# Optimization experiments

Hardware: AMD Instinct MI355X
Metric: run time of the kernel (lower is better)

## Reference

```python
import jax, jax.numpy as jnp
import numpy as np

N_NODES = 50000
N_EDGES = 800000
N_GRAPHS = 64
D_IN = 128
D_HID = 128
D_OUT = 32
N_LAYERS = 2


def setup_inputs() -> dict:
    key = jax.random.key(0)
    ks = jax.random.split(key, 12)
    x = jax.random.normal(ks[0], (N_NODES, D_IN), dtype=jnp.float32)
    edge_index = jax.random.randint(ks[1], (2, N_EDGES), 0, N_NODES, dtype=jnp.int64)
    batch = jnp.sort(jax.random.randint(ks[2], (N_NODES,), 0, N_GRAPHS, dtype=jnp.int64))
    s = 1.0 / np.sqrt(D_HID)
    return {
        "x": x,
        "edge_index": edge_index,
        "batch": batch,
        "conv_w_rel": jax.random.normal(ks[3], (N_LAYERS, D_IN, D_HID), dtype=jnp.float32) * s,
        "conv_b_rel": jax.random.normal(ks[4], (N_LAYERS, D_HID), dtype=jnp.float32) * s,
        "conv_w_root": jax.random.normal(ks[5], (N_LAYERS, D_IN, D_HID), dtype=jnp.float32) * s,
        "sage_w_l": jax.random.normal(ks[6], (N_LAYERS, D_HID, D_HID), dtype=jnp.float32) * s,
        "sage_b_l": jax.random.normal(ks[7], (N_LAYERS, D_HID), dtype=jnp.float32) * s,
        "sage_w_r": jax.random.normal(ks[8], (N_LAYERS, D_HID, D_HID), dtype=jnp.float32) * s,
        "fc_w": jax.random.normal(ks[9], (D_HID, D_OUT), dtype=jnp.float32) * s,
        "fc_b": jax.random.normal(ks[10], (D_OUT,), dtype=jnp.float32) * s,
    }


def reference(x, edge_index, batch, conv_w_rel, conv_b_rel, conv_w_root,
              sage_w_l, sage_b_l, sage_w_r, fc_w, fc_b):
    N = x.shape[0]
    src, dst = edge_index[0], edge_index[1]
    # StandardScaler: per-feature standardization (population std)
    mu = jnp.mean(x, axis=0)
    sd = jnp.std(x, axis=0)
    h = (x - mu) / sd
    # Stacked GraphConv layers: lin_rel(sum-aggr neighbors) + lin_root(x), then ReLU
    for l in range(conv_w_rel.shape[0]):
        agg = jax.ops.segment_sum(h[src], dst, num_segments=N)  # [N, D]
        h = jax.nn.relu(agg @ conv_w_rel[l] + conv_b_rel[l] + h @ conv_w_root[l])
    # GraphSAGE: SAGEConv layers (mean aggregation), ReLU between layers only
    deg = jax.ops.segment_sum(jnp.ones((src.shape[0],), dtype=h.dtype), dst, num_segments=N)
    deg = jnp.clip(deg, 1.0)[:, None]  # [N, 1]
    L = sage_w_l.shape[0]
    for l in range(L):
        agg = jax.ops.segment_sum(h[src], dst, num_segments=N) / deg  # mean over neighbors
        h_new = agg @ sage_w_l[l] + sage_b_l[l] + h @ sage_w_r[l]
        h = jax.nn.relu(h_new) if l < L - 1 else h_new
    # global_mean_pool over graphs
    sums = jax.ops.segment_sum(h, batch, num_segments=N_GRAPHS)  # [G, D]
    cnt = jax.ops.segment_sum(jnp.ones((N,), dtype=h.dtype), batch, num_segments=N_GRAPHS)
    pooled = sums / jnp.clip(cnt, 1.0)[:, None]
    return pooled @ fc_w + fc_b  # [G, D_OUT]
```

## Files before the change

kernel.cpp:

```cpp
#include <hip/hip_runtime.h>

#define N_NODES 50000
#define N_EDGES 800000
#define N_GRAPHS 64
#define DH 128
#define DOUT 32

typedef __attribute__((ext_vector_type(8))) short bf16x8;
typedef __attribute__((ext_vector_type(4))) float f32x4;

__device__ __forceinline__ unsigned short f2bf(float f) {
    union { float f; unsigned int u; } x;
    x.f = f;
    unsigned int u = x.u;
    u += 0x7FFFu + ((u >> 16) & 1u);
    return (unsigned short)(u >> 16);
}

#define STAT_BLKS 512
__global__ __launch_bounds__(256) void stats_kernel(const float* __restrict__ x,
                                                    float* __restrict__ partial) {
    __shared__ float4 shs[256];
    __shared__ float4 shq[256];
    const int tid = threadIdx.x;
    const int rowgrp = tid >> 5;
    const int cq = tid & 31;
    float4 s = make_float4(0.f, 0.f, 0.f, 0.f);
    float4 q = make_float4(0.f, 0.f, 0.f, 0.f);
#pragma unroll 4
    for (int r = blockIdx.x * 8 + rowgrp; r < N_NODES; r += STAT_BLKS * 8) {
        const float4 v = *reinterpret_cast<const float4*>(x + (size_t)r * DH + cq * 4);
        s.x += v.x; s.y += v.y; s.z += v.z; s.w += v.w;
        q.x = fmaf(v.x, v.x, q.x); q.y = fmaf(v.y, v.y, q.y);
        q.z = fmaf(v.z, v.z, q.z); q.w = fmaf(v.w, v.w, q.w);
    }
    shs[tid] = s; shq[tid] = q;
    __syncthreads();
    for (int off = 128; off >= 32; off >>= 1) {
        if (tid < off) {
            float4 a = shs[tid], b = shs[tid + off];
            a.x += b.x; a.y += b.y; a.z += b.z; a.w += b.w;
            shs[tid] = a;
            float4 c = shq[tid], d = shq[tid + off];
            c.x += d.x; c.y += d.y; c.z += d.z; c.w += d.w;
            shq[tid] = c;
        }
        __syncthreads();
    }
    if (tid < 32) {
        const float4 a = shs[tid];
        const float4 c = shq[tid];
        const float sv[4] = {a.x, a.y, a.z, a.w};
        const float qv[4] = {c.x, c.y, c.z, c.w};
#pragma unroll
        for (int j = 0; j < 4; ++j) {
            const int col = tid * 4 + j;
            partial[(size_t)col * STAT_BLKS + blockIdx.x] = sv[j];
            partial[(size_t)(128 + col) * STAT_BLKS + blockIdx.x] = qv[j];
        }
    }
}

__global__ __launch_bounds__(128) void finalize_stats_kernel(const float* __restrict__ partial,
                                                             float* __restrict__ stat) {
    const int c = threadIdx.x;
    const float4* ps = reinterpret_cast<const float4*>(partial + (size_t)c * STAT_BLKS);
    const float4* pq = reinterpret_cast<const float4*>(partial + (size_t)(128 + c) * STAT_BLKS);
    float s = 0.f, q = 0.f;
#pragma unroll 8
    for (int b = 0; b < STAT_BLKS / 4; ++b) {
        const float4 v = ps[b];
        s += v.x + v.y + v.z + v.w;
        const float4 w = pq[b];
        q += w.x + w.y + w.z + w.w;
    }
    const float inv_n = 1.0f / (float)N_NODES;
    const float mu = s * inv_n;
    const float var = q * inv_n - mu * mu;
    const float sd = sqrtf(fmaxf(var, 1e-20f));
    stat[256 + c] = mu;
    stat[384 + c] = 1.0f / sd;
}

__global__ void standardize_kernel(const float* __restrict__ x,
                                   const float* __restrict__ stat,
                                   unsigned short* __restrict__ h) {
    const size_t i = (size_t)blockIdx.x * blockDim.x + threadIdx.x;
    const int c4 = (int)(i & 31) << 2;
    const float4 v = reinterpret_cast<const float4*>(x)[i];
    const float4 m = *reinterpret_cast<const float4*>(stat + 256 + c4);
    const float4 is = *reinterpret_cast<const float4*>(stat + 384 + c4);
    ushort4 o;
    o.x = f2bf((v.x - m.x) * is.x);
    o.y = f2bf((v.y - m.y) * is.y);
    o.z = f2bf((v.z - m.z) * is.z);
    o.w = f2bf((v.w - m.w) * is.w);
    reinterpret_cast<ushort4*>(h)[i] = o;
}

__global__ void count_deg_kernel(const int* __restrict__ dst, int* __restrict__ deg_i) {
    int e = blockIdx.x * blockDim.x + threadIdx.x;
    if (e < N_EDGES) atomicAdd(&deg_i[dst[e]], 1);
}

#define SCAN_BLK 256
#define SCAN_NBLK ((N_NODES + SCAN_BLK - 1) / SCAN_BLK)

__global__ __launch_bounds__(SCAN_BLK) void scan_local_kernel(const int* __restrict__ deg_i,
                                                              int* __restrict__ row_ptr,
                                                              int* __restrict__ bsum) {
    __shared__ int sh[SCAN_BLK];
    const int tid = threadIdx.x;
    const int idx = blockIdx.x * SCAN_BLK + tid;
    const int v = (idx < N_NODES) ? deg_i[idx] : 0;
    sh[tid] = v;
    __syncthreads();
#pragma unroll
    for (int off = 1; off < SCAN_BLK; off <<= 1) {
        const int t = (tid >= off) ? sh[tid - off] : 0;
        __syncthreads();
        sh[tid] += t;
        __syncthreads();
    }
    if (idx < N_NODES) row_ptr[idx] = sh[tid] - v;
    if (tid == SCAN_BLK - 1) bsum[blockIdx.x] = sh[tid];
}

__global__ __launch_bounds__(SCAN_BLK) void scan_bsum_kernel(int* __restrict__ bsum) {
    __shared__ int sh[SCAN_BLK];
    const int tid = threadIdx.x;
    const int v = (tid < SCAN_NBLK) ? bsum[tid] : 0;
    sh[tid] = v;
    __syncthreads();
#pragma unroll
    for (int off = 1; off < SCAN_BLK; off <<= 1) {
        const int t = (tid >= off) ? sh[tid - off] : 0;
        __syncthreads();
        sh[tid] += t;
        __syncthreads();
    }
    if (tid < SCAN_NBLK) bsum[tid] = sh[tid] - v;
}

__global__ __launch_bounds__(SCAN_BLK) void scan_finalize_kernel(const int* __restrict__ deg_i,
                                                                 const int* __restrict__ bsum,
                                                                 int* __restrict__ row_ptr,
                                                                 int* __restrict__ cursor,
                                                                 float* __restrict__ deg_inv) {
    const int tid = threadIdx.x;
    const int idx = blockIdx.x * SCAN_BLK + tid;
    if (idx < N_NODES) {
        const int excl = row_ptr[idx] + bsum[blockIdx.x];
        row_ptr[idx] = excl;
        cursor[idx] = excl;
        const int d = deg_i[idx];
        deg_inv[idx] = 1.0f / (float)(d > 1 ? d : 1);
    }
    if (idx == 0) row_ptr[N_NODES] = N_EDGES;
}

#define NXCD 8
#define RANGE_NODES ((N_NODES + NXCD - 1) / NXCD)
#define SC_SLICES 104
__global__ __launch_bounds__(256) void scatter_ranged_kernel(const int* __restrict__ src,
                                                             const int* __restrict__ dst,
                                                             int* __restrict__ cursor,
                                                             int* __restrict__ csr_src) {
    const int range = blockIdx.x & (NXCD - 1);
    const int slice = blockIdx.x >> 3;
    const int lo = range * RANGE_NODES;
    const int hi = min(lo + RANGE_NODES, N_NODES);
    const int stride = SC_SLICES * 256;
    for (int e = slice * 256 + threadIdx.x; e < N_EDGES; e += stride) {
        const int d = dst[e];
        if (d >= lo && d < hi) {
            const int pos = atomicAdd(&cursor[d], 1);
            csr_src[pos] = src[e];
        }
    }
}

__global__ __launch_bounds__(256) void aggregate_csr_kernel(const unsigned short* __restrict__ h,
                                                            const int* __restrict__ row_ptr,
                                                            const int* __restrict__ csr_src,
                                                            const float* __restrict__ deg_inv,
                                                            unsigned short* __restrict__ agg,
                                                            const int useScale) {
    const int node = blockIdx.x * 4 + (threadIdx.x >> 6);
    if (node >= N_NODES) return;
    const int lane = threadIdx.x & 63;
    const int beg = row_ptr[node];
    const int end = row_ptr[node + 1];
    float a0 = 0.f, a1 = 0.f;
    for (int chunk = beg; chunk < end; chunk += 64) {
        const int cnt = min(64, end - chunk);
        const int sv = (lane < cnt) ? csr_src[chunk + lane] : 0;
        int j = 0;
        for (; j + 8 <= cnt; j += 8) {
            int ss[8];
#pragma unroll
            for (int u = 0; u < 8; ++u) ss[u] = __shfl(sv, j + u);
            unsigned int vv[8];
#pragma unroll
            for (int u = 0; u < 8; ++u)
                vv[u] = *reinterpret_cast<const unsigned int*>(h + (size_t)ss[u] * DH + lane * 2);
#pragma unroll
            for (int u = 0; u < 8; ++u) {
                union { unsigned int x; float f; } t;
                t.x = vv[u] << 16; a0 += t.f;
                t.x = vv[u] & 0xFFFF0000u; a1 += t.f;
            }
        }
        for (; j < cnt; ++j) {
            const int s = __shfl(sv, j);
            const unsigned int v = *reinterpret_cast<const unsigned int*>(h + (size_t)s * DH + lane * 2);
            union { unsigned int x; float f; } t;
            t.x = v << 16; a0 += t.f;
            t.x = v & 0xFFFF0000u; a1 += t.f;
        }
    }
    float o0 = a0, o1 = a1;
    if (useScale) {
        const float sc = deg_inv[node];
        o0 *= sc; o1 *= sc;
    }
    const unsigned int packed = (unsigned int)f2bf(o0) | ((unsigned int)f2bf(o1) << 16);
    reinterpret_cast<unsigned int*>(agg + (size_t)node * DH)[lane] = packed;
}

__global__ void pack_w_kernel(const float* __restrict__ cwr, const float* __restrict__ cwroot,
                              const float* __restrict__ swl, const float* __restrict__ swr,
                              unsigned short* __restrict__ wfrag) {
    const int g = blockIdx.x * blockDim.x + threadIdx.x;
    if (g >= 16384) return;
    const int lane = g & 63;
    const int n = (g >> 6) & 7;
    const int t = (g >> 9) & 3;
    const int phase = (g >> 11) & 1;
    const int layer = (g >> 12) & 3;
    const float* W1 = (layer < 2) ? (cwr + layer * 16384) : (swl + (layer - 2) * 16384);
    const float* W2 = (layer < 2) ? (cwroot + layer * 16384) : (swr + (layer - 2) * 16384);
    const float* W = phase ? W2 : W1;
    const int col = n * 16 + (lane & 15);
    const int k0 = t * 32 + (lane >> 4) * 8;
    unsigned short v[8];
#pragma unroll
    for (int j = 0; j < 8; ++j) v[j] = f2bf(W[(size_t)(k0 + j) * DH + col]);
    unsigned short* dstp = wfrag + ((size_t)g * 8);
#pragma unroll
    for (int j = 0; j < 8; ++j) dstp[j] = v[j];
}

__global__ __launch_bounds__(256) void fused_layer_mfma_kernel(
    const unsigned short* __restrict__ A1, const unsigned short* __restrict__ A2,
    const unsigned short* __restrict__ Wf, const float* __restrict__ bias,
    unsigned short* __restrict__ Cb, float* __restrict__ Cf, const int relu) {
    const int wid = threadIdx.x >> 6;
    const int lane = threadIdx.x & 63;
    const int row0 = blockIdx.x * 64 + wid * 16;
    const int arow = row0 + (lane & 15);
    const int koff = (lane >> 4) * 8;
    const bool rowOK = (arow < N_NODES);

    f32x4 acc[8];
#pragma unroll
    for (int n = 0; n < 8; ++n) acc[n] = (f32x4){0.f, 0.f, 0.f, 0.f};

#pragma unroll
    for (int phase = 0; phase < 2; ++phase) {
        const unsigned short* Ar = (phase ? A2 : A1) + (size_t)arow * DH;
        const unsigned short* Wp = Wf + (size_t)phase * (4 * 8 * 64 * 8);
#pragma unroll
        for (int t = 0; t < 4; ++t) {
            bf16x8 af = {};
            if (rowOK) af = *reinterpret_cast<const bf16x8*>(Ar + t * 32 + koff);
            const unsigned short* wt = Wp + (((size_t)t * 8) * 64 + lane) * 8;
#pragma unroll
            for (int n = 0; n < 8; ++n) {
                const bf16x8 bfv = *reinterpret_cast<const bf16x8*>(wt + (size_t)n * 64 * 8);
                acc[n] = __builtin_amdgcn_mfma_f32_16x16x32_bf16(af, bfv, acc[n], 0, 0, 0);
            }
        }
    }

    const int crow0 = row0 + (lane >> 4) * 4;
    const int ccol = lane & 15;
#pragma unroll
    for (int n = 0; n < 8; ++n) {
        const int col = n * 16 + ccol;
        const float bv = bias[col];
#pragma unroll
        for (int r = 0; r < 4; ++r) {
            const int grow = crow0 + r;
            if (grow >= N_NODES) continue;
            float v = acc[n][r] + bv;
            if (relu) {
                v = fmaxf(v, 0.f);
                Cb[(size_t)grow * DH + col] = f2bf(v);
            } else {
                Cf[(size_t)grow * DH + col] = v;
            }
        }
    }
}

#define POOL_BLOCKS 512
__global__ __launch_bounds__(128) void pool_seg_kernel(const float* __restrict__ h,
                                                       const int* __restrict__ batch,
                                                       float* __restrict__ pooled,
                                                       float* __restrict__ cnt) {
    const int c = threadIdx.x;
    const int nper = (N_NODES + POOL_BLOCKS - 1) / POOL_BLOCKS;
    const int n0 = blockIdx.x * nper;
    const int n1 = min(n0 + nper, N_NODES);
    if (n0 >= n1) return;
    float acc = 0.f;
    int g = batch[n0];
    int runlen = 0;
    for (int n = n0; n < n1; ++n) {
        const int bg = batch[n];
        if (bg != g) {
            atomicAdd(&pooled[(size_t)g * DH + c], acc);
            if (c == 0) atomicAdd(&cnt[g], (float)runlen);
            acc = 0.f; runlen = 0; g = bg;
        }
        acc += h[(size_t)n * DH + c];
        ++runlen;
    }
    atomicAdd(&pooled[(size_t)g * DH + c], acc);
    if (c == 0) atomicAdd(&cnt[g], (float)runlen);
}

__global__ void final_kernel(const float* __restrict__ pooled, const float* __restrict__ cnt,
                             const float* __restrict__ fcw, const float* __restrict__ fcb,
                             float* __restrict__ out) {
    const int g = blockIdx.x;
    const int j = threadIdx.x;
    if (j >= DOUT) return;
    const float inv = 1.0f / fmaxf(cnt[g], 1.0f);
    float acc = fcb[j];
    for (int d = 0; d < DH; ++d)
        acc = fmaf(pooled[(size_t)g * DH + d] * inv, fcw[(size_t)d * DOUT + j], acc);
    out[(size_t)g * DOUT + j] = acc;
}

extern "C" void kernel_launch(void* const* d_in, const int* in_sizes, int n_in,
                              void* d_out, int out_size, void* d_ws, size_t ws_size,
                              hipStream_t stream) {
    const float* x = (const float*)d_in[0];
    const int* ei = (const int*)d_in[1];
    const int* batch = (const int*)d_in[2];
    const float* conv_w_rel = (const float*)d_in[3];
    const float* conv_b_rel = (const float*)d_in[4];
    const float* conv_w_root = (const float*)d_in[5];
    const float* sage_w_l = (const float*)d_in[6];
    const float* sage_b_l = (const float*)d_in[7];
    const float* sage_w_r = (const float*)d_in[8];
    const float* fc_w = (const float*)d_in[9];
    const float* fc_b = (const float*)d_in[10];
    float* out = (float*)d_out;

    const int* src = ei;
    const int* dst = ei + N_EDGES;

    const size_t NHB = (size_t)N_NODES * DH * sizeof(unsigned short);
    const size_t NFB = (size_t)N_NODES * DH * sizeof(float);
    char* p = (char*)d_ws;
    unsigned short* hb0 = (unsigned short*)p; p += NHB;
    unsigned short* hb1 = (unsigned short*)p; p += NHB;
    unsigned short* aggb = (unsigned short*)p; p += NHB;
    float* hF = (float*)p; p += NFB;
    float* deg_inv = (float*)p; p += ((size_t)N_NODES * sizeof(float) + 255) & ~(size_t)255;
    float* stat = (float*)p; p += 512 * sizeof(float);
    float* pooled = (float*)p; p += (size_t)N_GRAPHS * DH * sizeof(float);
    float* cnt = (float*)p; p += ((size_t)N_GRAPHS * sizeof(float) + 255) & ~(size_t)255;
    int* deg_i = (int*)p; p += ((size_t)N_NODES * sizeof(int) + 255) & ~(size_t)255;
    int* row_ptr = (int*)p; p += ((size_t)(N_NODES + 1) * sizeof(int) + 255) & ~(size_t)255;
    int* cursor = (int*)p; p += ((size_t)N_NODES * sizeof(int) + 255) & ~(size_t)255;
    int* bsum = (int*)p; p += ((size_t)SCAN_BLK * sizeof(int) + 255) & ~(size_t)255;
    float* partial = (float*)p; p += (size_t)256 * STAT_BLKS * sizeof(float);
    unsigned short* wfrag = (unsigned short*)p; p += (size_t)4 * 32768 * sizeof(unsigned short);
    int* csr_src = (int*)p; p += (size_t)N_EDGES * sizeof(int);

    hipLaunchKernelGGL(stats_kernel, dim3(STAT_BLKS), dim3(256), 0, stream, x, partial);
    hipLaunchKernelGGL(finalize_stats_kernel, dim3(1), dim3(DH), 0, stream, partial, stat);
    hipLaunchKernelGGL(standardize_kernel, dim3((N_NODES * DH / 4) / 256), dim3(256), 0, stream,
                       x, stat, hb0);

    hipLaunchKernelGGL(pack_w_kernel, dim3(64), dim3(256), 0, stream,
                       conv_w_rel, conv_w_root, sage_w_l, sage_w_r, wfrag);

    hipMemsetAsync(deg_i, 0, (size_t)N_NODES * sizeof(int), stream);
    hipLaunchKernelGGL(count_deg_kernel, dim3((N_EDGES + 255) / 256), dim3(256), 0, stream,
                       dst, deg_i);
    hipLaunchKernelGGL(scan_local_kernel, dim3(SCAN_NBLK), dim3(SCAN_BLK), 0, stream,
                       deg_i, row_ptr, bsum);
    hipLaunchKernelGGL(scan_bsum_kernel, dim3(1), dim3(SCAN_BLK), 0, stream, bsum);
    hipLaunchKernelGGL(scan_finalize_kernel, dim3(SCAN_NBLK), dim3(SCAN_BLK), 0, stream,
                       deg_i, bsum, row_ptr, cursor, deg_inv);
    hipLaunchKernelGGL(scatter_ranged_kernel, dim3(NXCD * SC_SLICES), dim3(256), 0, stream,
                       src, dst, cursor, csr_src);

    const float* Bs[4] = {conv_b_rel, conv_b_rel + 128, sage_b_l, sage_b_l + 128};

    unsigned short* curb = hb0;
    unsigned short* nxtb = hb1;
    const dim3 aggGrid((N_NODES + 3) / 4);
    const dim3 gemmGrid((N_NODES + 63) / 64);
    for (int l = 0; l < 4; ++l) {
        hipLaunchKernelGGL(aggregate_csr_kernel, aggGrid, dim3(256), 0, stream,
                           curb, row_ptr, csr_src, deg_inv, aggb, (l >= 2) ? 1 : 0);
        hipLaunchKernelGGL(fused_layer_mfma_kernel, gemmGrid, dim3(256), 0, stream,
                           aggb, curb, wfrag + (size_t)l * 32768, Bs[l],
                           (l < 3) ? nxtb : (unsigned short*)nullptr,
                           (l < 3) ? (float*)nullptr : hF,
                           (l < 3) ? 1 : 0);
        unsigned short* t = curb; curb = nxtb; nxtb = t;
    }

    hipMemsetAsync(pooled, 0, ((size_t)N_GRAPHS * DH + N_GRAPHS) * sizeof(float), stream);
    hipLaunchKernelGGL(pool_seg_kernel, dim3(POOL_BLOCKS), dim3(DH), 0, stream,
                       hF, batch, pooled, cnt);
    hipLaunchKernelGGL(final_kernel, dim3(N_GRAPHS), dim3(64), 0, stream,
                       pooled, cnt, fc_w, fc_b, out);
}
```

Baseline: 358.4 us.

## Split CSR aggregation across column quarters with four edges per wavefront step

The aggregation kernel now launches four blocks per node group along blockIdx.y, each handling a 32-column quarter of the feature row. Within a wavefront, four groups of 16 lanes each fetch a different neighbor's 64-byte slice, and the partial sums are combined with cross-lane xor shuffles before one group writes the result. This aims to raise parallelism and memory-level concurrency for low-degree nodes. In exchange it drops the 8-way unrolled batching of loads, quadruples the reads of row_ptr and csr_src, and uses narrower 64-byte gathers per neighbor.

```diff
diff --git a/kernel.cpp b/kernel.cpp
--- a/kernel.cpp
+++ b/kernel.cpp
@@ -188,7 +188,11 @@
                                                             const int useScale) {
     const int node = blockIdx.x * 4 + (threadIdx.x >> 6);
     if (node >= N_NODES) return;
+    const int q = blockIdx.y;
     const int lane = threadIdx.x & 63;
+    const int grp = lane >> 4;
+    const int cp = lane & 15;
+    const int coff = q * 32 + cp * 2;
     const int beg = row_ptr[node];
     const int end = row_ptr[node + 1];
     float a0 = 0.f, a1 = 0.f;
@@ -196,36 +200,35 @@
         const int cnt = min(64, end - chunk);
         const int sv = (lane < cnt) ? csr_src[chunk + lane] : 0;
         int j = 0;
-        for (; j + 8 <= cnt; j += 8) {
-            int ss[8];
-#pragma unroll
-            for (int u = 0; u < 8; ++u) ss[u] = __shfl(sv, j + u);
-            unsigned int vv[8];
-#pragma unroll
-            for (int u = 0; u < 8; ++u)
-                vv[u] = *reinterpret_cast<const unsigned int*>(h + (size_t)ss[u] * DH + lane * 2);
-#pragma unroll
-            for (int u = 0; u < 8; ++u) {
-                union { unsigned int x; float f; } t;
-                t.x = vv[u] << 16; a0 += t.f;
-                t.x = vv[u] & 0xFFFF0000u; a1 += t.f;
-            }
-        }
-        for (; j < cnt; ++j) {
-            const int s = __shfl(sv, j);
-            const unsigned int v = *reinterpret_cast<const unsigned int*>(h + (size_t)s * DH + lane * 2);
+        for (; j + 4 <= cnt; j += 4) {
+            const int s = __shfl(sv, j + grp);
+            const unsigned int v = *reinterpret_cast<const unsigned int*>(h + (size_t)s * DH + coff);
             union { unsigned int x; float f; } t;
             t.x = v << 16; a0 += t.f;
             t.x = v & 0xFFFF0000u; a1 += t.f;
         }
-    }
-    float o0 = a0, o1 = a1;
-    if (useScale) {
-        const float sc = deg_inv[node];
-        o0 *= sc; o1 *= sc;
-    }
-    const unsigned int packed = (unsigned int)f2bf(o0) | ((unsigned int)f2bf(o1) << 16);
-    reinterpret_cast<unsigned int*>(agg + (size_t)node * DH)[lane] = packed;
+        const int rem = cnt - j;
+        if (rem > 0) {
+            const int s = __shfl(sv, j + grp);
+            if (grp < rem) {
+                const unsigned int v = *reinterpret_cast<const unsigned int*>(h + (size_t)s * DH + coff);
+                union { unsigned int x; float f; } t;
+                t.x = v << 16; a0 += t.f;
+                t.x = v & 0xFFFF0000u; a1 += t.f;
+            }
+        }
+    }
+    a0 += __shfl_xor(a0, 16); a0 += __shfl_xor(a0, 32);
+    a1 += __shfl_xor(a1, 16); a1 += __shfl_xor(a1, 32);
+    if (lane < 16) {
+        float o0 = a0, o1 = a1;
+        if (useScale) {
+            const float sc = deg_inv[node];
+            o0 *= sc; o1 *= sc;
+        }
+        const unsigned int packed = (unsigned int)f2bf(o0) | ((unsigned int)f2bf(o1) << 16);
+        reinterpret_cast<unsigned int*>(agg + (size_t)node * DH + q * 32)[cp] = packed;
+    }
 }
 
 __global__ void pack_w_kernel(const float* __restrict__ cwr, const float* __restrict__ cwroot,
@@ -405,7 +408,7 @@
 
     unsigned short* curb = hb0;
     unsigned short* nxtb = hb1;
-    const dim3 aggGrid((N_NODES + 3) / 4);
+    const dim3 aggGrid((N_NODES + 3) / 4, 4);
     const dim3 gemmGrid((N_NODES + 63) / 64);
     for (int l = 0; l < 4; ++l) {
         hipLaunchKernelGGL(aggregate_csr_kernel, aggGrid, dim3(256), 0, stream,
```

After: 561.0 us. 1.57x slower.
